# Kernel optimization log

Measured on AMD Instinct MI355X. Metric: run time of the kernel, lower is better.

The kernel has to match this reference:

```python
import jax, jax.numpy as jnp
import numpy as np

B, T, D, H, F = 2, 2048, 1024, 16, 4096
DH = D // H  # 64
EPS = 1e-5


def setup_inputs() -> dict:
    key = jax.random.key(0)
    ks = jax.random.split(key, 12)
    s = 0.02
    return {
        "embedding": jax.random.normal(ks[0], (B, T, D), dtype=jnp.float32),
        "Wq": jax.random.normal(ks[1], (H, D, DH), dtype=jnp.float32) * s,
        "Wk": jax.random.normal(ks[2], (H, D, DH), dtype=jnp.float32) * s,
        "Wv": jax.random.normal(ks[3], (H, D, DH), dtype=jnp.float32) * s,
        "Wo": jax.random.normal(ks[4], (D, D), dtype=jnp.float32) * s,
        "bo": jnp.zeros((D,), dtype=jnp.float32),
        "W1": jax.random.normal(ks[5], (D, F), dtype=jnp.float32) * s,
        "b1": jnp.zeros((F,), dtype=jnp.float32),
        "W2": jax.random.normal(ks[6], (F, D), dtype=jnp.float32) * s,
        "b2": jnp.zeros((D,), dtype=jnp.float32),
        "g1": jnp.ones((D,), dtype=jnp.float32),
        "be1": jnp.zeros((D,), dtype=jnp.float32),
        "g2": jnp.ones((D,), dtype=jnp.float32),
        "be2": jnp.zeros((D,), dtype=jnp.float32),
    }


def _layernorm(x, g, b):
    mu = jnp.mean(x, axis=-1, keepdims=True)
    var = jnp.mean(jnp.square(x - mu), axis=-1, keepdims=True)
    return (x - mu) * jax.lax.rsqrt(var + EPS) * g + b


def reference(embedding, Wq, Wk, Wv, Wo, bo, W1, b1, W2, b2, g1, be1, g2, be2):
    x = embedding  # [B, T, D]
    # per-head projections (no bias), stacked: [B, H, T, DH]
    q = jnp.einsum("btd,hde->bhte", x, Wq)
    k = jnp.einsum("btd,hde->bhte", x, Wk)
    v = jnp.einsum("btd,hde->bhte", x, Wv)
    scores = jnp.einsum("bhte,bhse->bhts", q, k)  # [B, H, T, T]
    mask = jnp.tril(jnp.ones((T, T), dtype=bool))
    # Original masks to -inf first, then scales; -inf * scale = -inf, so this
    # equals softmax(scale * scores) on the causal support.
    scale = DH ** (-0.5)
    scores = jnp.where(mask, scores * scale, -jnp.inf)
    attn = jax.nn.softmax(scores, axis=-1)
    o = jnp.einsum("bhts,bhse->bthe", attn, v).reshape(B, T, D)  # head concat
    attn_out = o @ Wo + bo
    a = x + _layernorm(attn_out, g1, be1)  # residual uses original input
    f = jax.nn.relu(a @ W1 + b1) @ W2 + b2
    out = x + _layernorm(f, g2, be2)  # NOTE: residual from x, as in source
    return out
```

## Files before the change

kernel.cpp:

```cpp
#include <hip/hip_runtime.h>
#include <hip/hip_bf16.h>


#define Bq_ 2
#define T_ 2048
#define D_ 1024
#define H_ 16
#define DH_ 64
#define F_ 4096
#define N_ (Bq_ * T_)
#define EPS_ 1e-5f
#define KP 72

typedef __hip_bfloat16 bf16;
typedef unsigned short u16;
typedef __attribute__((ext_vector_type(8))) short bfrag;
typedef __attribute__((ext_vector_type(4))) float f32x4;

__device__ __forceinline__ u16 f2b(float f) {
    bf16 h = __float2bfloat16(f);
    return *(u16*)&h;
}
__device__ __forceinline__ float b2f_bits(u16 u) {
    return __uint_as_float(((unsigned)u) << 16);
}

__device__ __forceinline__ int swz(int row, int col) {
    return (col & ~31) | ((((col >> 3) ^ (row >> 1)) & 3) << 3) | (col & 7);
}

template <int N>
__device__ __forceinline__ void vmwait() {
    asm volatile("s_waitcnt vmcnt(%0)" :: "i"(N) : "memory");
}

#define GLDS16(g, l) __builtin_amdgcn_global_load_lds( \
    (const __attribute__((address_space(1))) unsigned int*)(g), \
    (__attribute__((address_space(3))) unsigned int*)(l), 16, 0, 0)

__device__ __forceinline__ void xcd_remap(int gx, int& bx, int& by) {
    const int bid = blockIdx.x + gx * blockIdx.y;
    const int t8 = bid >> 3;
    bx = t8 % gx;
    by = (bid & 7) + 8 * (t8 / gx);
}

__device__ __forceinline__ void tc_body(
    float (*Ts)[65], const float* s, int spitch,
    u16* dst, int dpitch, int drow0, int kcol0)
{
    const int t = threadIdx.x;
    #pragma unroll
    for (int i = 0; i < 4; i++) {
        const int idx = t + i * 256;
        const int kk = idx >> 4;
        const int mm = (idx & 15) * 4;
        float4 v = *(const float4*)(s + (size_t)kk * spitch + mm);
        Ts[mm][kk] = v.x; Ts[mm + 1][kk] = v.y;
        Ts[mm + 2][kk] = v.z; Ts[mm + 3][kk] = v.w;
    }
    __syncthreads();
    const int mm = t >> 2;
    const int kk0 = (t & 3) * 16;
    u16 o[16];
    #pragma unroll
    for (int j = 0; j < 16; j++) o[j] = f2b(Ts[mm][kk0 + j]);
    const int dr = drow0 + mm;
    u16* drow = dst + (size_t)dr * dpitch;
    const int c0 = kcol0 + kk0;
    *(uint4*)&drow[swz(dr, c0)]     = *(uint4*)&o[0];
    *(uint4*)&drow[swz(dr, c0 + 8)] = *(uint4*)&o[8];
}

__global__ __launch_bounds__(256) void tcvt(
    const float* __restrict__ src, int spitch, int srow0, int scol0,
    u16* __restrict__ dst, int dpitch, int drow0)
{
    __shared__ float Ts[64][65];
    const int mb = blockIdx.x, kb = blockIdx.y;
    const float* s = src + (size_t)(srow0 + kb * 64) * spitch + scol0 + mb * 64;
    tc_body(Ts, s, spitch, dst, dpitch, drow0 + mb * 64, kb * 64);
}

__global__ __launch_bounds__(256) void tcvt_kv(
    const float* __restrict__ Wk, const float* __restrict__ Wv,
    u16* __restrict__ dst)
{
    __shared__ float Ts[64][65];
    const int kb = blockIdx.y, z = blockIdx.z;
    const int sel = z >> 4, zz = z & 15;
    const float* src = sel ? Wv : Wk;
    const float* s = src + (size_t)zz * 1024 * 64 + (size_t)(kb * 64) * 64;
    tc_body(Ts, s, 64, dst, 1024, sel * 1024 + zz * 64, kb * 64);
}

__global__ __launch_bounds__(256) void tcvt_ffn(
    const float* __restrict__ W1, const float* __restrict__ W2, int c,
    u16* __restrict__ W1T, u16* __restrict__ W2T)
{
    __shared__ float Ts[64][65];
    const int mb = blockIdx.x, kb = blockIdx.y, z = blockIdx.z;
    const float* src = z ? W2 : W1;
    const int spitch = z ? 1024 : 4096;
    const int srow0  = z ? c * 1024 : 0;
    const int scol0  = z ? 0 : c * 1024;
    u16* dst = z ? W2T : W1T;
    const float* s = src + (size_t)(srow0 + kb * 64) * spitch + scol0 + mb * 64;
    tc_body(Ts, s, spitch, dst, 1024, mb * 64, kb * 64);
}

template <int AF32, int SPLIT, int RELU, int ACC, int NT, int CSWZ, int WAVE>
__global__ __launch_bounds__(256) void cgemm(
    const void* __restrict__ A, int lda,
    const u16* __restrict__ BT,
    u16* __restrict__ C0, u16* __restrict__ C1, int ldc,
    int Kdim,
    const float* __restrict__ bias, int bias_off)
{
    static_assert(NT == 2 || NT == 4, "NT");
    static_assert(!AF32 || NT == 4, "AF32 path assumes BN=128");
    static_assert(!(AF32 && WAVE), "WAVE requires glds-only staging");
    constexpr int BN = NT * 32;
    constexpr int NBUF = (NT == 2) ? 5 : 4;
    constexpr int DPT  = NBUF - 1;
    constexpr int LPT  = 4 + NT;
    constexpr int BELEM = 64 * 32;
    constexpr int AELEM = NT * 16 * 32;
    constexpr int PBUF  = BELEM + AELEM;
    constexpr int SELEM = WAVE ? 4 * NBUF * PBUF
                               : 2 * BN * 32 + 2 * 128 * 32;
    __shared__ alignas(16) u16 SMEM[SELEM];

    const int tid = threadIdx.x;
    const int lane = tid & 63;
    const int w = tid >> 6;
    const int lo16 = lane & 15;
    const int quad = lane >> 4;
    const int wi = w >> 1, wj = w & 1;

    int bx, by;
    xcd_remap(gridDim.x, bx, by);
    const int m0 = bx * 128;
    const int n0 = by * BN;

    f32x4 acc[NT][4] = {};

    const int c8 = (lane & 3) * 8;
    const int r4 = lane >> 2;
    const int fcol = ((quad ^ ((lo16 >> 1) & 3)) << 3);

    const int nsteps = Kdim >> 5;

    if constexpr (WAVE) {
        const u16* Ab = (const u16*)A;
        u16* wbase = &SMEM[w * NBUF * PBUF];
        auto wstage = [&](int slot, int k0) {
            u16* bb = wbase + slot * PBUF;
            #pragma unroll
            for (int c = 0; c < 4; c++)
                GLDS16(BT + (size_t)(m0 + wj * 64 + c * 16 + r4) * Kdim + k0 + c8,
                       bb + c * 512);
            u16* ab = bb + BELEM;
            #pragma unroll
            for (int c = 0; c < NT; c++)
                GLDS16(Ab + (size_t)(n0 + wi * (NT * 16) + c * 16 + r4) * lda + k0 + c8,
                       ab + c * 512);
        };
        #pragma unroll
        for (int i = 0; i < DPT; i++) wstage(i, i * 32);
        int t = 0, cb = 0;
        for (; t + DPT <= nsteps; ++t) {
            vmwait<(DPT - 1) * LPT>();
            __builtin_amdgcn_sched_barrier(0);
            const u16* bb = wbase + cb * PBUF;
            const u16* ab = bb + BELEM;
            bfrag af[NT], bfv[4];
            #pragma unroll
            for (int it = 0; it < NT; it++)
                af[it] = *(const bfrag*)(ab + (it * 16 + lo16) * 32 + fcol);
            #pragma unroll
            for (int jt = 0; jt < 4; jt++)
                bfv[jt] = *(const bfrag*)(bb + (jt * 16 + lo16) * 32 + fcol);
            if (t + DPT < nsteps)
                wstage(cb == 0 ? NBUF - 1 : cb - 1, (t + DPT) * 32);
            __builtin_amdgcn_s_setprio(1);
            #pragma unroll
            for (int it = 0; it < NT; it++)
                #pragma unroll
                for (int jt = 0; jt < 4; jt++)
                    acc[it][jt] = __builtin_amdgcn_mfma_f32_16x16x32_bf16(
                        af[it], bfv[jt], acc[it][jt], 0, 0, 0);
            __builtin_amdgcn_s_setprio(0);
            cb = (cb + 1 == NBUF) ? 0 : cb + 1;
        }
        vmwait<0>();
        __builtin_amdgcn_sched_barrier(0);
        for (; t < nsteps; ++t) {
            const u16* bb = wbase + cb * PBUF;
            const u16* ab = bb + BELEM;
            bfrag af[NT], bfv[4];
            #pragma unroll
            for (int it = 0; it < NT; it++)
                af[it] = *(const bfrag*)(ab + (it * 16 + lo16) * 32 + fcol);
            #pragma unroll
            for (int jt = 0; jt < 4; jt++)
                bfv[jt] = *(const bfrag*)(bb + (jt * 16 + lo16) * 32 + fcol);
            #pragma unroll
            for (int it = 0; it < NT; it++)
                #pragma unroll
                for (int jt = 0; jt < 4; jt++)
                    acc[it][jt] = __builtin_amdgcn_mfma_f32_16x16x32_bf16(
                        af[it], bfv[jt], acc[it][jt], 0, 0, 0);
            cb = (cb + 1 == NBUF) ? 0 : cb + 1;
        }
    } else {
        u16* As_ = SMEM;
        u16* Bs_ = SMEM + 2 * BN * 32;
        const int br0 = w * 32 + r4;
        const int br1 = br0 + 16;
        auto stage = [&](int buf, int k0) {
            GLDS16(BT + (size_t)(m0 + br0) * Kdim + k0 + c8,
                   Bs_ + buf * 128 * 32 + (w * 2 + 0) * 512);
            GLDS16(BT + (size_t)(m0 + br1) * Kdim + k0 + c8,
                   Bs_ + buf * 128 * 32 + (w * 2 + 1) * 512);
            const int ar = tid >> 1;
            const int kh = (tid & 1) * 16;
            const float* ap = (const float*)A + (size_t)(n0 + ar) * lda + k0 + kh;
            float4 v0 = ((const float4*)ap)[0];
            float4 v1 = ((const float4*)ap)[1];
            float4 v2 = ((const float4*)ap)[2];
            float4 v3 = ((const float4*)ap)[3];
            uint4 a0, a1;
            a0.x = (unsigned)f2b(v0.x) | ((unsigned)f2b(v0.y) << 16);
            a0.y = (unsigned)f2b(v0.z) | ((unsigned)f2b(v0.w) << 16);
            a0.z = (unsigned)f2b(v1.x) | ((unsigned)f2b(v1.y) << 16);
            a0.w = (unsigned)f2b(v1.z) | ((unsigned)f2b(v1.w) << 16);
            a1.x = (unsigned)f2b(v2.x) | ((unsigned)f2b(v2.y) << 16);
            a1.y = (unsigned)f2b(v2.z) | ((unsigned)f2b(v2.w) << 16);
            a1.z = (unsigned)f2b(v3.x) | ((unsigned)f2b(v3.y) << 16);
            a1.w = (unsigned)f2b(v3.z) | ((unsigned)f2b(v3.w) << 16);
            u16* arow = As_ + buf * BN * 32 + ar * 32;
            *(uint4*)&arow[swz(ar, kh)] = a0;
            *(uint4*)&arow[swz(ar, kh + 8)] = a1;
        };
        stage(0, 0);
        __syncthreads();
        int cur = 0;
        for (int t = 0; t < nsteps; ++t) {
            if (t + 1 < nsteps) stage(cur ^ 1, (t + 1) * 32);
            bfrag af[NT], bfv[4];
            #pragma unroll
            for (int it = 0; it < NT; it++)
                af[it] = *(const bfrag*)(As_ + cur * BN * 32
                         + (wi * (NT * 16) + it * 16 + lo16) * 32 + fcol);
            #pragma unroll
            for (int jt = 0; jt < 4; jt++)
                bfv[jt] = *(const bfrag*)(Bs_ + cur * 128 * 32
                          + (wj * 64 + jt * 16 + lo16) * 32 + fcol);
            __builtin_amdgcn_s_setprio(1);
            #pragma unroll
            for (int it = 0; it < NT; it++)
                #pragma unroll
                for (int jt = 0; jt < 4; jt++)
                    acc[it][jt] = __builtin_amdgcn_mfma_f32_16x16x32_bf16(
                        af[it], bfv[jt], acc[it][jt], 0, 0, 0);
            __builtin_amdgcn_s_setprio(0);
            if (t + 1 < nsteps) {
                __syncthreads();
                cur ^= 1;
            }
        }
    }
    #pragma unroll
    for (int jt = 0; jt < 4; jt++) {
        const int col = m0 + wj * 64 + jt * 16 + lo16;
        u16* Cp;
        int cc;
        if constexpr (SPLIT) {
            Cp = (col >> 10) ? C1 : C0;
            cc = col & 1023;
        } else {
            Cp = C0;
            cc = col;
        }
        const float bv = bias ? bias[bias_off + col] : 0.f;
        #pragma unroll
        for (int it = 0; it < NT; it++) {
            #pragma unroll
            for (int r = 0; r < 4; r++) {
                const int row = n0 + wi * (NT * 16) + it * 16 + quad * 4 + r;
                float v = acc[it][jt][r] + bv;
                if constexpr (RELU) v = fmaxf(v, 0.f);
                const int ccs = CSWZ ? swz(row, cc) : cc;
                u16* cp = Cp + (size_t)row * ldc + ccs;
                if constexpr (ACC) v += b2f_bits(*cp);
                *cp = f2b(v);
            }
        }
    }
}

template <int AF32, int QKV, int RELU, int ACC>
__global__ __launch_bounds__(256) void mgemm(
    const void* __restrict__ A,
    const float* __restrict__ B0f, const float* __restrict__ B1f, const float* __restrict__ B2f,
    u16* __restrict__ C0, u16* __restrict__ C1, u16* __restrict__ C2,
    int ldb, int brow_off, int bcol_off,
    const float* __restrict__ bias, int bias_off)
{
    __shared__ alignas(16) u16 As[128][32];
    __shared__ alignas(16) u16 Bt[128][40];
    __shared__ alignas(16) float Bs32[32][132];

    const int tid = threadIdx.x;
    const int lane = tid & 63;
    const int w = tid >> 6;
    const int lo16 = lane & 15;
    const int quad = lane >> 4;
    const int wi = w >> 1, wj = w & 1;

    int bx, by;
    xcd_remap(gridDim.x, bx, by);
    const int m0 = bx * 128;
    const int n0 = by * 128;

    f32x4 acc[4][4] = {};

    const int ar  = tid >> 1;
    const int akh = (tid & 1) * 16;
    const int bmq = tid & 31;
    const int bkb = (tid >> 5) * 4;
    const int tm  = tid >> 1;
    const int tkh = (tid & 1) * 16;

    for (int k0 = 0; k0 < 1024; k0 += 32) {
        uint4 a0, a1;
        if constexpr (AF32) {
            const float* ap = (const float*)A + (size_t)(n0 + ar) * 1024 + k0 + akh;
            float4 v0 = ((const float4*)ap)[0];
            float4 v1 = ((const float4*)ap)[1];
            float4 v2 = ((const float4*)ap)[2];
            float4 v3 = ((const float4*)ap)[3];
            a0.x = (unsigned)f2b(v0.x) | ((unsigned)f2b(v0.y) << 16);
            a0.y = (unsigned)f2b(v0.z) | ((unsigned)f2b(v0.w) << 16);
            a0.z = (unsigned)f2b(v1.x) | ((unsigned)f2b(v1.y) << 16);
            a0.w = (unsigned)f2b(v1.z) | ((unsigned)f2b(v1.w) << 16);
            a1.x = (unsigned)f2b(v2.x) | ((unsigned)f2b(v2.y) << 16);
            a1.y = (unsigned)f2b(v2.z) | ((unsigned)f2b(v2.w) << 16);
            a1.z = (unsigned)f2b(v3.x) | ((unsigned)f2b(v3.y) << 16);
            a1.w = (unsigned)f2b(v3.z) | ((unsigned)f2b(v3.w) << 16);
        } else {
            const u16* ap = (const u16*)A + (size_t)(n0 + ar) * 1024 + k0 + akh;
            a0 = ((const uint4*)ap)[0];
            a1 = ((const uint4*)ap)[1];
        }
        #pragma unroll
        for (int kk = 0; kk < 4; kk++) {
            const int k = bkb + kk;
            const float* bp;
            if constexpr (QKV) {
                const int m = m0 + bmq * 4;
                const int sel = m >> 10;
                const int mm = m & 1023;
                const float* Wp = (sel == 0) ? B0f : ((sel == 1) ? B1f : B2f);
                bp = Wp + ((size_t)(mm >> 6) * 1024 + k0 + k) * 64 + (mm & 63);
            } else {
                bp = B0f + (size_t)(brow_off + k0 + k) * ldb + bcol_off + m0 + bmq * 4;
            }
            *(float4*)&Bs32[k][bmq * 4] = *(const float4*)bp;
        }
        __syncthreads();
        *(uint4*)&As[ar][akh] = a0;
        *(uint4*)&As[ar][akh + 8] = a1;
        {
            u16 t[16];
            #pragma unroll
            for (int i = 0; i < 16; i++) t[i] = f2b(Bs32[tkh + i][tm]);
            *(uint4*)&Bt[tm][tkh] = *(uint4*)&t[0];
            *(uint4*)&Bt[tm][tkh + 8] = *(uint4*)&t[8];
        }
        __syncthreads();
        bfrag af[4], bfv[4];
        #pragma unroll
        for (int it = 0; it < 4; it++)
            af[it] = *(const bfrag*)&As[wi * 64 + it * 16 + lo16][quad * 8];
        #pragma unroll
        for (int jt = 0; jt < 4; jt++)
            bfv[jt] = *(const bfrag*)&Bt[wj * 64 + jt * 16 + lo16][quad * 8];
        #pragma unroll
        for (int it = 0; it < 4; it++)
            #pragma unroll
            for (int jt = 0; jt < 4; jt++)
                acc[it][jt] = __builtin_amdgcn_mfma_f32_16x16x32_bf16(
                    af[it], bfv[jt], acc[it][jt], 0, 0, 0);
        __syncthreads();
    }
    #pragma unroll
    for (int jt = 0; jt < 4; jt++) {
        const int col = m0 + wj * 64 + jt * 16 + lo16;
        u16* Cp;
        int cc;
        if constexpr (QKV) {
            const int sel = col >> 10;
            cc = col & 1023;
            Cp = (sel == 0) ? C0 : ((sel == 1) ? C1 : C2);
        } else {
            Cp = C0;
            cc = col;
        }
        const float bv = bias ? bias[bias_off + col] : 0.f;
        #pragma unroll
        for (int it = 0; it < 4; it++) {
            #pragma unroll
            for (int r = 0; r < 4; r++) {
                const int row = n0 + wi * 64 + it * 16 + quad * 4 + r;
                float v = acc[it][jt][r] + bv;
                if constexpr (RELU) v = fmaxf(v, 0.f);
                u16* cp = Cp + (size_t)row * 1024 + cc;
                if constexpr (ACC) v += b2f_bits(*cp);
                *cp = f2b(v);
            }
        }
    }
}

__global__ __launch_bounds__(256) void fattn_kernel(
    u16* __restrict__ Q, const u16* __restrict__ Kg, const u16* __restrict__ Vg)
{
    const int bi = blockIdx.x;
    const int qp = bi & 15;
    const int h  = (bi >> 4) & 15;
    const int b  = bi >> 8;
    const int tid = threadIdx.x;
    const int w = tid >> 6;
    const int lane = tid & 63;
    const int lo16 = lane & 15;
    const int quad = lane >> 4;

    __shared__ alignas(16) u16 Ks[64][KP];
    __shared__ alignas(16) u16 Vt[64][KP];
    __shared__ alignas(16) u16 Ps[4][16][KP];

    const int sr = tid >> 2;
    const int ec = (tid & 3) * 16;

    #pragma unroll 1
    for (int pi = 0; pi < 2; pi++) {
        const int qt = pi ? (31 - qp) : qp;
        const int q0 = qt * 64;
        const size_t qrow = (size_t)(b * T_ + q0 + w * 16 + lo16) * 1024 + h * 64;
        bfrag qa0 = *(const bfrag*)(Q + qrow + quad * 8);
        bfrag qa1 = *(const bfrag*)(Q + qrow + 32 + quad * 8);

        f32x4 oacc[4] = {};
        float m_r[4], l_r[4];
        #pragma unroll
        for (int r = 0; r < 4; r++) { m_r[r] = -3e38f; l_r[r] = 0.f; }

        uint4 ka, kb, va, vb;
        {
            const size_t grow = (size_t)(b * T_ + sr) * 1024 + h * 64 + ec;
            ka = *(const uint4*)(Kg + grow);
            kb = *(const uint4*)(Kg + grow + 8);
            va = *(const uint4*)(Vg + grow);
            vb = *(const uint4*)(Vg + grow + 8);
        }

        for (int st = 0; st <= qt; st++) {
            *(uint4*)&Ks[sr][ec] = ka;
            *(uint4*)&Ks[sr][ec + 8] = kb;
            {
                unsigned vv[8] = {va.x, va.y, va.z, va.w, vb.x, vb.y, vb.z, vb.w};
                #pragma unroll
                for (int k2 = 0; k2 < 8; k2++) {
                    Vt[ec + 2 * k2][sr]     = (u16)(vv[k2] & 0xffff);
                    Vt[ec + 2 * k2 + 1][sr] = (u16)(vv[k2] >> 16);
                }
            }
            __syncthreads();
            if (st < qt) {
                const size_t grow = (size_t)(b * T_ + (st + 1) * 64 + sr) * 1024
                                  + h * 64 + ec;
                ka = *(const uint4*)(Kg + grow);
                kb = *(const uint4*)(Kg + grow + 8);
                va = *(const uint4*)(Vg + grow);
                vb = *(const uint4*)(Vg + grow + 8);
            }

            float sv[4][4];
            #pragma unroll
            for (int nt = 0; nt < 4; nt++) {
                bfrag kb0 = *(const bfrag*)&Ks[nt * 16 + lo16][quad * 8];
                bfrag kb1 = *(const bfrag*)&Ks[nt * 16 + lo16][32 + quad * 8];
                f32x4 cs = {0.f, 0.f, 0.f, 0.f};
                cs = __builtin_amdgcn_mfma_f32_16x16x32_bf16(qa0, kb0, cs, 0, 0, 0);
                cs = __builtin_amdgcn_mfma_f32_16x16x32_bf16(qa1, kb1, cs, 0, 0, 0);
                #pragma unroll
                for (int r = 0; r < 4; r++) sv[nt][r] = cs[r] * 0.125f;
            }
            if (st == qt) {
                #pragma unroll
                for (int nt = 0; nt < 4; nt++)
                    #pragma unroll
                    for (int r = 0; r < 4; r++)
                        if (nt * 16 + lo16 > w * 16 + quad * 4 + r) sv[nt][r] = -3e38f;
            }
            #pragma unroll
            for (int r = 0; r < 4; r++) {
                float m = fmaxf(fmaxf(sv[0][r], sv[1][r]), fmaxf(sv[2][r], sv[3][r]));
                #pragma unroll
                for (int off = 1; off < 16; off <<= 1)
                    m = fmaxf(m, __shfl_xor(m, off, 64));
                float mnew = fmaxf(m_r[r], m);
                float alpha = __expf(m_r[r] - mnew);
                m_r[r] = mnew;
                float s = 0.f;
                #pragma unroll
                for (int nt = 0; nt < 4; nt++) {
                    sv[nt][r] = __expf(sv[nt][r] - mnew);
                    s += sv[nt][r];
                }
                #pragma unroll
                for (int off = 1; off < 16; off <<= 1)
                    s += __shfl_xor(s, off, 64);
                l_r[r] = l_r[r] * alpha + s;
                #pragma unroll
                for (int et = 0; et < 4; et++) oacc[et][r] *= alpha;
            }
            #pragma unroll
            for (int nt = 0; nt < 4; nt++)
                #pragma unroll
                for (int r = 0; r < 4; r++)
                    Ps[w][quad * 4 + r][nt * 16 + lo16] = f2b(sv[nt][r]);
            bfrag pa0 = *(const bfrag*)&Ps[w][lo16][quad * 8];
            bfrag pa1 = *(const bfrag*)&Ps[w][lo16][32 + quad * 8];
            #pragma unroll
            for (int et = 0; et < 4; et++) {
                bfrag vb0 = *(const bfrag*)&Vt[et * 16 + lo16][quad * 8];
                bfrag vb1 = *(const bfrag*)&Vt[et * 16 + lo16][32 + quad * 8];
                oacc[et] = __builtin_amdgcn_mfma_f32_16x16x32_bf16(pa0, vb0, oacc[et], 0, 0, 0);
                oacc[et] = __builtin_amdgcn_mfma_f32_16x16x32_bf16(pa1, vb1, oacc[et], 0, 0, 0);
            }
            __syncthreads();
        }
        #pragma unroll
        for (int r = 0; r < 4; r++) {
            float rl = 1.f / l_r[r];
            const int row = q0 + w * 16 + quad * 4 + r;
            u16* orow = Q + (size_t)(b * T_ + row) * 1024;
            #pragma unroll
            for (int et = 0; et < 4; et++)
                orow[swz(row, h * 64 + et * 16 + lo16)] = f2b(oacc[et][r] * rl);
        }
    }
}

template <int WF32, int OSWZ>
__global__ __launch_bounds__(256) void ln_kernel(
    const u16* __restrict__ src, const float* __restrict__ resid,
    const float* __restrict__ g, const float* __restrict__ be,
    u16* __restrict__ dstb, float* __restrict__ dstf)
{
    const int r = blockIdx.x;
    const int tid = threadIdx.x;
    uint2 raw = ((const uint2*)(src + (size_t)r * D_))[tid];
    float y[4];
    y[0] = __uint_as_float(raw.x << 16);
    y[1] = __uint_as_float(raw.x & 0xffff0000u);
    y[2] = __uint_as_float(raw.y << 16);
    y[3] = __uint_as_float(raw.y & 0xffff0000u);
    float s = y[0] + y[1] + y[2] + y[3];
    float sq = y[0]*y[0] + y[1]*y[1] + y[2]*y[2] + y[3]*y[3];
    #pragma unroll
    for (int o = 32; o > 0; o >>= 1) {
        s += __shfl_down(s, o, 64);
        sq += __shfl_down(sq, o, 64);
    }
    __shared__ float rs[4], rq[4];
    if ((tid & 63) == 0) { rs[tid >> 6] = s; rq[tid >> 6] = sq; }
    __syncthreads();
    const float S = rs[0] + rs[1] + rs[2] + rs[3];
    const float Qm = rq[0] + rq[1] + rq[2] + rq[3];
    const float mu = S * (1.f / (float)D_);
    const float var = fmaxf(Qm * (1.f / (float)D_) - mu * mu, 0.f);
    const float rstd = rsqrtf(var + EPS_);
    const int c = tid * 4;
    #pragma unroll
    for (int i = 0; i < 4; i++) {
        y[i] = (y[i] - mu) * rstd * g[c + i] + be[c + i]
             + resid[(size_t)r * D_ + c + i];
    }
    if constexpr (WF32) {
        float4 o = {y[0], y[1], y[2], y[3]};
        ((float4*)(dstf + (size_t)r * D_))[tid] = o;
    } else {
        uint2 o;
        o.x = (unsigned)f2b(y[0]) | ((unsigned)f2b(y[1]) << 16);
        o.y = (unsigned)f2b(y[2]) | ((unsigned)f2b(y[3]) << 16);
        const int cs = OSWZ ? swz(r, c) : c;
        *(uint2*)(dstb + (size_t)r * D_ + cs) = o;
    }
}

extern "C" void kernel_launch(void* const* d_in, const int* in_sizes, int n_in,
                              void* d_out, int out_size, void* d_ws, size_t ws_size,
                              hipStream_t stream)
{
    const float* emb = (const float*)d_in[0];
    const float* Wq  = (const float*)d_in[1];
    const float* Wk  = (const float*)d_in[2];
    const float* Wv  = (const float*)d_in[3];
    const float* Wo  = (const float*)d_in[4];
    const float* bo  = (const float*)d_in[5];
    const float* W1  = (const float*)d_in[6];
    const float* b1  = (const float*)d_in[7];
    const float* W2  = (const float*)d_in[8];
    const float* b2  = (const float*)d_in[9];
    const float* g1  = (const float*)d_in[10];
    const float* be1 = (const float*)d_in[11];
    const float* g2  = (const float*)d_in[12];
    const float* be2 = (const float*)d_in[13];

    u16* WS = (u16*)d_ws;
    u16* DO = (u16*)d_out;

    const size_t M1 = 1024 * 1024;
    u16* WkvT = WS;
    u16* Q    = WS;
    u16* Kb   = DO;
    u16* Vb   = DO + 4 * M1;
    u16* O    = WS;
    u16* WoT  = DO;
    u16* P    = DO + 4 * M1;
    u16* Af   = DO;
    u16* Hc   = DO + 4 * M1;
    u16* W1T  = DO + 6 * M1;
    u16* W2T  = DO + 7 * M1;
    u16* F    = WS;
    float* outf = (float*)d_out;

    const dim3 blk(256);

    tcvt_kv<<<dim3(1, 16, 32), blk, 0, stream>>>(Wk, Wv, WkvT);
    cgemm<1, 1, 0, 0, 4, 0, 0><<<dim3(16, 32), blk, 0, stream>>>(
        emb, 1024, WkvT, Kb, Vb, 1024, 1024, nullptr, 0);
    mgemm<1, 1, 0, 0><<<dim3(8, 32), blk, 0, stream>>>(
        emb, Wq, Wq, Wq, Q, nullptr, nullptr, 0, 0, 0, nullptr, 0);
    fattn_kernel<<<Bq_ * H_ * 16, blk, 0, stream>>>(Q, Kb, Vb);
    tcvt<<<dim3(16, 16), blk, 0, stream>>>(Wo, 1024, 0, 0, WoT, 1024, 0);
    cgemm<0, 0, 0, 0, 4, 0, 1><<<dim3(8, 32), blk, 0, stream>>>(
        O, 1024, WoT, P, nullptr, 1024, 1024, bo, 0);
    ln_kernel<0, 1><<<N_, blk, 0, stream>>>(P, emb, g1, be1, Af, nullptr);
    for (int c = 0; c < 4; c++) {
        tcvt_ffn<<<dim3(16, 16, 2), blk, 0, stream>>>(W1, W2, c, W1T, W2T);
        for (int rh = 0; rh < 2; rh++) {
            u16* Afh = Af + (size_t)rh * 2048 * 1024;
            u16* Fh  = F  + (size_t)rh * 2048 * 1024;
            cgemm<0, 0, 1, 0, 2, 1, 1><<<dim3(8, 32), blk, 0, stream>>>(
                Afh, 1024, W1T, Hc, nullptr, 1024, 1024, b1, c * 1024);
            if (c == 0) {
                cgemm<0, 0, 0, 0, 2, 0, 1><<<dim3(8, 32), blk, 0, stream>>>(
                    Hc, 1024, W2T, Fh, nullptr, 1024, 1024, b2, 0);
            } else {
                cgemm<0, 0, 0, 1, 2, 0, 1><<<dim3(8, 32), blk, 0, stream>>>(
                    Hc, 1024, W2T, Fh, nullptr, 1024, 1024, nullptr, 0);
            }
        }
    }
    ln_kernel<1, 0><<<N_, blk, 0, stream>>>(F, emb, g2, be2, nullptr, outf);
}
```

Baseline: 548.0 us.

## Write V transposed from KV GEMM epilogue and drop attention-side transpose

The KV projection GEMM now stores the V half in a transposed [B, head-dim, T] layout, using packed 4-element stores along T. The attention kernel then loads V rows straight into the Vt shared tile with vector stores, replacing the per-element scattered LDS transpose. This is meant to cut LDS bank conflicts and instruction count in the attention inner loop, which runs many times per block. In exchange the GEMM epilogue writes V with a strided pattern.

```diff
diff --git a/kernel.cpp b/kernel.cpp
--- a/kernel.cpp
+++ b/kernel.cpp
@@ -109,7 +109,7 @@
     tc_body(Ts, s, spitch, dst, 1024, mb * 64, kb * 64);
 }
 
-template <int AF32, int SPLIT, int RELU, int ACC, int NT, int CSWZ, int WAVE>
+template <int AF32, int SPLIT, int RELU, int ACC, int NT, int CSWZ, int WAVE, int VT>
 __global__ __launch_bounds__(256) void cgemm(
     const void* __restrict__ A, int lda,
     const u16* __restrict__ BT,
@@ -120,6 +120,7 @@
     static_assert(NT == 2 || NT == 4, "NT");
     static_assert(!AF32 || NT == 4, "AF32 path assumes BN=128");
     static_assert(!(AF32 && WAVE), "WAVE requires glds-only staging");
+    static_assert(!VT || SPLIT, "VT requires SPLIT");
     constexpr int BN = NT * 32;
     constexpr int NBUF = (NT == 2) ? 5 : 4;
     constexpr int DPT  = NBUF - 1;
@@ -274,27 +275,33 @@
     #pragma unroll
     for (int jt = 0; jt < 4; jt++) {
         const int col = m0 + wj * 64 + jt * 16 + lo16;
-        u16* Cp;
-        int cc;
-        if constexpr (SPLIT) {
-            Cp = (col >> 10) ? C1 : C0;
-            cc = col & 1023;
+        const bool vhalf = SPLIT && (col >> 10);
+        const int cc = SPLIT ? (col & 1023) : col;
+        if (VT && vhalf) {
+            #pragma unroll
+            for (int it = 0; it < NT; it++) {
+                const int rowb = n0 + wi * (NT * 16) + it * 16 + quad * 4;
+                u16 pk[4];
+                #pragma unroll
+                for (int r = 0; r < 4; r++) pk[r] = f2b(acc[it][jt][r]);
+                *(uint2*)(C1 + ((size_t)((rowb >> 11) * 1024 + cc)) * 2048
+                          + (rowb & 2047)) = *(uint2*)pk;
+            }
         } else {
-            Cp = C0;
-            cc = col;
-        }
-        const float bv = bias ? bias[bias_off + col] : 0.f;
-        #pragma unroll
-        for (int it = 0; it < NT; it++) {
-            #pragma unroll
-            for (int r = 0; r < 4; r++) {
-                const int row = n0 + wi * (NT * 16) + it * 16 + quad * 4 + r;
-                float v = acc[it][jt][r] + bv;
-                if constexpr (RELU) v = fmaxf(v, 0.f);
-                const int ccs = CSWZ ? swz(row, cc) : cc;
-                u16* cp = Cp + (size_t)row * ldc + ccs;
-                if constexpr (ACC) v += b2f_bits(*cp);
-                *cp = f2b(v);
+            u16* Cp = vhalf ? C1 : C0;
+            const float bv = bias ? bias[bias_off + col] : 0.f;
+            #pragma unroll
+            for (int it = 0; it < NT; it++) {
+                #pragma unroll
+                for (int r = 0; r < 4; r++) {
+                    const int row = n0 + wi * (NT * 16) + it * 16 + quad * 4 + r;
+                    float v = acc[it][jt][r] + bv;
+                    if constexpr (RELU) v = fmaxf(v, 0.f);
+                    const int ccs = CSWZ ? swz(row, cc) : cc;
+                    u16* cp = Cp + (size_t)row * ldc + ccs;
+                    if constexpr (ACC) v += b2f_bits(*cp);
+                    *cp = f2b(v);
+                }
             }
         }
     }
@@ -443,6 +450,7 @@
 
     const int sr = tid >> 2;
     const int ec = (tid & 3) * 16;
+    const size_t vrow = ((size_t)(b * 1024 + h * 64 + sr)) * 2048;
 
     #pragma unroll 1
     for (int pi = 0; pi < 2; pi++) {
@@ -462,29 +470,23 @@
             const size_t grow = (size_t)(b * T_ + sr) * 1024 + h * 64 + ec;
             ka = *(const uint4*)(Kg + grow);
             kb = *(const uint4*)(Kg + grow + 8);
-            va = *(const uint4*)(Vg + grow);
-            vb = *(const uint4*)(Vg + grow + 8);
+            va = *(const uint4*)(Vg + vrow + ec);
+            vb = *(const uint4*)(Vg + vrow + ec + 8);
         }
 
         for (int st = 0; st <= qt; st++) {
             *(uint4*)&Ks[sr][ec] = ka;
             *(uint4*)&Ks[sr][ec + 8] = kb;
-            {
-                unsigned vv[8] = {va.x, va.y, va.z, va.w, vb.x, vb.y, vb.z, vb.w};
-                #pragma unroll
-                for (int k2 = 0; k2 < 8; k2++) {
-                    Vt[ec + 2 * k2][sr]     = (u16)(vv[k2] & 0xffff);
-                    Vt[ec + 2 * k2 + 1][sr] = (u16)(vv[k2] >> 16);
-                }
-            }
+            *(uint4*)&Vt[sr][ec] = va;
+            *(uint4*)&Vt[sr][ec + 8] = vb;
             __syncthreads();
             if (st < qt) {
                 const size_t grow = (size_t)(b * T_ + (st + 1) * 64 + sr) * 1024
                                   + h * 64 + ec;
                 ka = *(const uint4*)(Kg + grow);
                 kb = *(const uint4*)(Kg + grow + 8);
-                va = *(const uint4*)(Vg + grow);
-                vb = *(const uint4*)(Vg + grow + 8);
+                va = *(const uint4*)(Vg + vrow + (st + 1) * 64 + ec);
+                vb = *(const uint4*)(Vg + vrow + (st + 1) * 64 + ec + 8);
             }
 
             float sv[4][4];
@@ -642,13 +644,13 @@
     const dim3 blk(256);
 
     tcvt_kv<<<dim3(1, 16, 32), blk, 0, stream>>>(Wk, Wv, WkvT);
-    cgemm<1, 1, 0, 0, 4, 0, 0><<<dim3(16, 32), blk, 0, stream>>>(
+    cgemm<1, 1, 0, 0, 4, 0, 0, 1><<<dim3(16, 32), blk, 0, stream>>>(
         emb, 1024, WkvT, Kb, Vb, 1024, 1024, nullptr, 0);
     mgemm<1, 1, 0, 0><<<dim3(8, 32), blk, 0, stream>>>(
         emb, Wq, Wq, Wq, Q, nullptr, nullptr, 0, 0, 0, nullptr, 0);
     fattn_kernel<<<Bq_ * H_ * 16, blk, 0, stream>>>(Q, Kb, Vb);
     tcvt<<<dim3(16, 16), blk, 0, stream>>>(Wo, 1024, 0, 0, WoT, 1024, 0);
-    cgemm<0, 0, 0, 0, 4, 0, 1><<<dim3(8, 32), blk, 0, stream>>>(
+    cgemm<0, 0, 0, 0, 4, 0, 1, 0><<<dim3(8, 32), blk, 0, stream>>>(
         O, 1024, WoT, P, nullptr, 1024, 1024, bo, 0);
     ln_kernel<0, 1><<<N_, blk, 0, stream>>>(P, emb, g1, be1, Af, nullptr);
     for (int c = 0; c < 4; c++) {
@@ -656,13 +658,13 @@
         for (int rh = 0; rh < 2; rh++) {
             u16* Afh = Af + (size_t)rh * 2048 * 1024;
             u16* Fh  = F  + (size_t)rh * 2048 * 1024;
-            cgemm<0, 0, 1, 0, 2, 1, 1><<<dim3(8, 32), blk, 0, stream>>>(
+            cgemm<0, 0, 1, 0, 2, 1, 1, 0><<<dim3(8, 32), blk, 0, stream>>>(
                 Afh, 1024, W1T, Hc, nullptr, 1024, 1024, b1, c * 1024);
             if (c == 0) {
-                cgemm<0, 0, 0, 0, 2, 0, 1><<<dim3(8, 32), blk, 0, stream>>>(
+                cgemm<0, 0, 0, 0, 2, 0, 1, 0><<<dim3(8, 32), blk, 0, stream>>>(
                     Hc, 1024, W2T, Fh, nullptr, 1024, 1024, b2, 0);
             } else {
-                cgemm<0, 0, 0, 1, 2, 0, 1><<<dim3(8, 32), blk, 0, stream>>>(
+                cgemm<0, 0, 0, 1, 2, 0, 1, 0><<<dim3(8, 32), blk, 0, stream>>>(
                     Hc, 1024, W2T, Fh, nullptr, 1024, 1024, nullptr, 0);
             }
         }
```

New measurement: 535.4 us. -2.3%, faster.
